# Optimization experiments

Measured on AMD Instinct MI355X. Metric: run time of the kernel, lower is better.

Reference implementation:

```python
import jax, jax.numpy as jnp
import numpy as np
import math

B, L, D, NUM_TYPES = 4, 4096, 512, 22
T_MAX = 200.0
SIGMA, LAMBD = 10.0, 0.005


def setup_inputs() -> dict:
    key = jax.random.key(0)
    k1, k2, k3 = jax.random.split(key, 3)
    event_type = jax.random.randint(k1, (B, L), 0, NUM_TYPES + 1)
    # event times in [0, t_max), sorted along the sequence (realistic point process)
    event_time = jnp.sort(jax.random.uniform(k2, (B, L), dtype=jnp.float32) * T_MAX, axis=-1)
    # embedding table with padding row 0 zeroed (padding_idx=0)
    emb_table = jax.random.normal(k3, (NUM_TYPES + 1, D), dtype=jnp.float32).at[0].set(0.0)
    return {"event_type": event_type, "event_time": event_time, "emb_table": emb_table}


def reference(event_type, event_time, emb_table):
    d_model = emb_table.shape[1]
    seq_len = event_time.shape[1]

    # sinusoidal temporal encoding: t / 10000^(2*(i//2)/d)
    i = jnp.arange(d_model)
    pos_vec = jnp.power(jnp.float32(10000.0), 2.0 * (i // 2).astype(jnp.float32) / d_model)
    temp = event_time[:, :, None] / pos_vec  # [B, L, D]
    temp_enc = jnp.where(i % 2 == 0, jnp.sin(temp), jnp.cos(temp))

    type_embedding = emb_table[event_type] * math.sqrt(d_model)  # [B, L, D]
    embedding = jnp.concatenate([temp_enc, type_embedding], axis=-1)  # [B, L, 2D]

    # RBF kernel pairwise scores: sigma^2 * exp(-(|ti - tj|^norm)^2 / lambd^2), norm=2
    t = event_time / T_MAX  # normalized times
    d = jnp.abs(t[:, :, None] - t[:, None, :]) ** 2  # [B, L, L]
    scores = (SIGMA ** 2) * jnp.exp(-(d ** 2) / (LAMBD ** 2))

    # causal mask: keep j <= i, fill future with -1000, then softmax over rows
    causal = jnp.tril(jnp.ones((seq_len, seq_len), dtype=bool))  # [L, L]
    scores = jnp.where(causal[None, :, :], scores, jnp.float32(-1000.0))
    scores = jax.nn.softmax(scores, axis=-1)
    return scores, embedding
```

## Files before the change

### kernel.cpp

```cpp
#include <hip/hip_runtime.h>

#define SEQ_L 4096
#define BATCH 4
#define DMODEL 512
#define ROWS_PER_BLOCK 4
#define CUT 0.055f

__global__ __launch_bounds__(256) void scores_kernel(const float* __restrict__ tm,
                                                     float* __restrict__ out) {
    __shared__ float ts[SEQ_L];

    const int b  = blockIdx.x / (SEQ_L / ROWS_PER_BLOCK);
    const int i0 = (blockIdx.x % (SEQ_L / ROWS_PER_BLOCK)) * ROWS_PER_BLOCK;

    const float4* tb4 = (const float4*)(tm + b * SEQ_L);
    float4* ts4 = (float4*)ts;
    for (int j = threadIdx.x; j < SEQ_L / 4; j += 256) {
        float4 v = tb4[j];
        v.x /= 200.0f; v.y /= 200.0f; v.z /= 200.0f; v.w /= 200.0f;
        ts4[j] = v;
    }
    __syncthreads();

    const int wave = threadIdx.x >> 6;
    const int lane = threadIdx.x & 63;
    const int i = i0 + wave;
    const float ti = ts[i];
    const float tcut = ti - CUT;

    int lo = 0, hi = i;
    while (lo < hi) {
        int mid = (lo + hi) >> 1;
        if (ts[mid] < tcut) lo = mid + 1; else hi = mid;
    }
    const int jlo = lo;

    float sum = 0.0f;
    for (int j = jlo + lane; j <= i; j += 64) {
        float d = ti - ts[j];
        float d2 = d * d;
        float s = 100.0f * expf(-(d2 * d2) * 40000.0f);
        sum += expf(s - 100.0f);
    }
    #pragma unroll
    for (int off = 1; off < 64; off <<= 1) sum += __shfl_xor(sum, off, 64);
    const float inv_denom = 1.0f / sum;

    float4* out4 = (float4*)(out + ((size_t)(b * SEQ_L + i)) * SEQ_L);
    for (int c = lane; c < SEQ_L / 4; c += 64) {
        const int j = c * 4;
        float4 v = make_float4(0.0f, 0.0f, 0.0f, 0.0f);
        if (j + 3 >= jlo && j <= i) {
            float* vp = &v.x;
            #pragma unroll
            for (int q = 0; q < 4; ++q) {
                const int jj = j + q;
                if (jj >= jlo && jj <= i) {
                    float d = ti - ts[jj];
                    float d2 = d * d;
                    float s = 100.0f * expf(-(d2 * d2) * 40000.0f);
                    vp[q] = expf(s - 100.0f) * inv_denom;
                }
            }
        }
        out4[c] = v;
    }
}

__global__ __launch_bounds__(256) void emb_kernel(const int* __restrict__ et,
                                                  const float* __restrict__ tm,
                                                  const float* __restrict__ tab,
                                                  float* __restrict__ out) {
    const int t = threadIdx.x;
    const bool temporal = t < 128;

    float ipA = 0.0f, ipB = 0.0f;
    if (temporal) {
        const float c = -13.287712379549449f / 256.0f;
        ipA = exp2f(c * (float)(2 * t));
        ipB = exp2f(c * (float)(2 * t + 1));
    }
    const int ecol = (t - 128) * 4;

    for (int bl = blockIdx.x; bl < BATCH * SEQ_L; bl += gridDim.x) {
        float4 v;
        if (temporal) {
            const float time = tm[bl];
            const float a = time * ipA;
            const float bph = time * ipB;
            v.x = sinf(a);  v.y = cosf(a);
            v.z = sinf(bph); v.w = cosf(bph);
        } else {
            const float4 e = *(const float4*)(tab + et[bl] * DMODEL + ecol);
            const float sc = 22.627416997969522f;
            v.x = e.x * sc; v.y = e.y * sc; v.z = e.z * sc; v.w = e.w * sc;
        }
        ((float4*)(out + (size_t)bl * 2 * DMODEL))[t] = v;
    }
}

extern "C" void kernel_launch(void* const* d_in, const int* in_sizes, int n_in,
                              void* d_out, int out_size, void* d_ws, size_t ws_size,
                              hipStream_t stream) {
    const int*   event_type = (const int*)d_in[0];
    const float* event_time = (const float*)d_in[1];
    const float* emb_table  = (const float*)d_in[2];

    float* scores = (float*)d_out;
    float* emb    = scores + (size_t)BATCH * SEQ_L * SEQ_L;

    scores_kernel<<<BATCH * SEQ_L / ROWS_PER_BLOCK, 256, 0, stream>>>(event_time, scores);
    emb_kernel<<<2048, 256, 0, stream>>>(event_type, event_time, emb_table, emb);
}
```

Baseline: 67.47 us.

## Fuse scores and embedding kernels, process 16 rows per block with fast math

Merges the scores and embedding kernels into a single launch that splits its blocks by index. Each score block now handles 16 rows, with each wave doing 4 consecutive rows, so the shared time array is loaded once for more rows and the window start is advanced incrementally instead of searched for every row. It also switches expf/sinf/cosf to the fast __expf/__sinf/__cosf intrinsics. The aim is to cut the cost of a second launch and of repeated shared-memory loads, at the risk of lower accuracy from the intrinsics and fewer blocks to spread across the device.

```diff
diff --git a/kernel.cpp b/kernel.cpp
--- a/kernel.cpp
+++ b/kernel.cpp
@@ -3,99 +3,115 @@
 #define SEQ_L 4096
 #define BATCH 4
 #define DMODEL 512
-#define ROWS_PER_BLOCK 4
 #define CUT 0.055f
+#define RPB 16
+#define SCORE_BLOCKS (BATCH * SEQ_L / RPB)
+#define EMB_BLOCKS 512
+#define EMB_RPB (BATCH * SEQ_L / EMB_BLOCKS)
 
-__global__ __launch_bounds__(256) void scores_kernel(const float* __restrict__ tm,
-                                                     float* __restrict__ out) {
-    __shared__ float ts[SEQ_L];
+__global__ __launch_bounds__(256) void fused_kernel(const int* __restrict__ et,
+                                                    const float* __restrict__ tm,
+                                                    const float* __restrict__ tab,
+                                                    float* __restrict__ scores,
+                                                    float* __restrict__ emb) {
+    if (blockIdx.x < SCORE_BLOCKS) {
+        __shared__ float ts[SEQ_L];
+        const int b  = blockIdx.x / (SEQ_L / RPB);
+        const int i0 = (blockIdx.x % (SEQ_L / RPB)) * RPB;
 
-    const int b  = blockIdx.x / (SEQ_L / ROWS_PER_BLOCK);
-    const int i0 = (blockIdx.x % (SEQ_L / ROWS_PER_BLOCK)) * ROWS_PER_BLOCK;
+        const float4* tb4 = (const float4*)(tm + b * SEQ_L);
+        float4* ts4 = (float4*)ts;
+        const float inv_tmax = 1.0f / 200.0f;
+        #pragma unroll
+        for (int q = 0; q < 4; ++q) {
+            int j = threadIdx.x + q * 256;
+            float4 v = tb4[j];
+            v.x *= inv_tmax; v.y *= inv_tmax; v.z *= inv_tmax; v.w *= inv_tmax;
+            ts4[j] = v;
+        }
+        __syncthreads();
 
-    const float4* tb4 = (const float4*)(tm + b * SEQ_L);
-    float4* ts4 = (float4*)ts;
-    for (int j = threadIdx.x; j < SEQ_L / 4; j += 256) {
-        float4 v = tb4[j];
-        v.x /= 200.0f; v.y /= 200.0f; v.z /= 200.0f; v.w /= 200.0f;
-        ts4[j] = v;
-    }
-    __syncthreads();
+        const int wave = threadIdx.x >> 6;
+        const int lane = threadIdx.x & 63;
+        const int ibase = i0 + wave * 4;
 
-    const int wave = threadIdx.x >> 6;
-    const int lane = threadIdx.x & 63;
-    const int i = i0 + wave;
-    const float ti = ts[i];
-    const float tcut = ti - CUT;
+        int jlo;
+        {
+            const float tc = ts[ibase] - CUT;
+            int lo = 0, hi = ibase;
+            while (lo < hi) {
+                int mid = (lo + hi) >> 1;
+                if (ts[mid] < tc) lo = mid + 1; else hi = mid;
+            }
+            jlo = lo;
+        }
 
-    int lo = 0, hi = i;
-    while (lo < hi) {
-        int mid = (lo + hi) >> 1;
-        if (ts[mid] < tcut) lo = mid + 1; else hi = mid;
-    }
-    const int jlo = lo;
+        for (int r = 0; r < 4; ++r) {
+            const int i = ibase + r;
+            const float ti = ts[i];
+            const float tc = ti - CUT;
+            while (ts[jlo] < tc) ++jlo;
 
-    float sum = 0.0f;
-    for (int j = jlo + lane; j <= i; j += 64) {
-        float d = ti - ts[j];
-        float d2 = d * d;
-        float s = 100.0f * expf(-(d2 * d2) * 40000.0f);
-        sum += expf(s - 100.0f);
-    }
-    #pragma unroll
-    for (int off = 1; off < 64; off <<= 1) sum += __shfl_xor(sum, off, 64);
-    const float inv_denom = 1.0f / sum;
+            float sum = 0.0f;
+            for (int j = jlo + lane; j <= i; j += 64) {
+                float d = ti - ts[j];
+                float d2 = d * d;
+                float s = 100.0f * __expf(-(d2 * d2) * 40000.0f);
+                sum += __expf(s - 100.0f);
+            }
+            #pragma unroll
+            for (int off = 1; off < 64; off <<= 1) sum += __shfl_xor(sum, off, 64);
+            const float inv_denom = 1.0f / sum;
 
-    float4* out4 = (float4*)(out + ((size_t)(b * SEQ_L + i)) * SEQ_L);
-    for (int c = lane; c < SEQ_L / 4; c += 64) {
-        const int j = c * 4;
-        float4 v = make_float4(0.0f, 0.0f, 0.0f, 0.0f);
-        if (j + 3 >= jlo && j <= i) {
-            float* vp = &v.x;
-            #pragma unroll
-            for (int q = 0; q < 4; ++q) {
-                const int jj = j + q;
-                if (jj >= jlo && jj <= i) {
-                    float d = ti - ts[jj];
-                    float d2 = d * d;
-                    float s = 100.0f * expf(-(d2 * d2) * 40000.0f);
-                    vp[q] = expf(s - 100.0f) * inv_denom;
+            float4* out4 = (float4*)(scores + ((size_t)(b * SEQ_L + i)) * SEQ_L);
+            for (int c = lane; c < SEQ_L / 4; c += 64) {
+                const int j = c * 4;
+                float4 v = make_float4(0.0f, 0.0f, 0.0f, 0.0f);
+                if (j + 3 >= jlo && j <= i) {
+                    float* vp = &v.x;
+                    #pragma unroll
+                    for (int q = 0; q < 4; ++q) {
+                        const int jj = j + q;
+                        if (jj >= jlo && jj <= i) {
+                            float d = ti - ts[jj];
+                            float d2 = d * d;
+                            float s = 100.0f * __expf(-(d2 * d2) * 40000.0f);
+                            vp[q] = __expf(s - 100.0f) * inv_denom;
+                        }
+                    }
                 }
+                out4[c] = v;
             }
         }
-        out4[c] = v;
-    }
-}
+    } else {
+        const int t = threadIdx.x;
+        const bool temporal = t < 128;
 
-__global__ __launch_bounds__(256) void emb_kernel(const int* __restrict__ et,
-                                                  const float* __restrict__ tm,
-                                                  const float* __restrict__ tab,
-                                                  float* __restrict__ out) {
-    const int t = threadIdx.x;
-    const bool temporal = t < 128;
+        float ipA = 0.0f, ipB = 0.0f;
+        if (temporal) {
+            const float c = -13.287712379549449f / 256.0f;
+            ipA = exp2f(c * (float)(2 * t));
+            ipB = exp2f(c * (float)(2 * t + 1));
+        }
+        const int ecol = (t - 128) * 4;
 
-    float ipA = 0.0f, ipB = 0.0f;
-    if (temporal) {
-        const float c = -13.287712379549449f / 256.0f;
-        ipA = exp2f(c * (float)(2 * t));
-        ipB = exp2f(c * (float)(2 * t + 1));
-    }
-    const int ecol = (t - 128) * 4;
-
-    for (int bl = blockIdx.x; bl < BATCH * SEQ_L; bl += gridDim.x) {
-        float4 v;
-        if (temporal) {
-            const float time = tm[bl];
-            const float a = time * ipA;
-            const float bph = time * ipB;
-            v.x = sinf(a);  v.y = cosf(a);
-            v.z = sinf(bph); v.w = cosf(bph);
-        } else {
-            const float4 e = *(const float4*)(tab + et[bl] * DMODEL + ecol);
-            const float sc = 22.627416997969522f;
-            v.x = e.x * sc; v.y = e.y * sc; v.z = e.z * sc; v.w = e.w * sc;
+        const int bl0 = (blockIdx.x - SCORE_BLOCKS) * EMB_RPB;
+        for (int r = 0; r < EMB_RPB; ++r) {
+            const int bl = bl0 + r;
+            float4 v;
+            if (temporal) {
+                const float time = tm[bl];
+                const float a = time * ipA;
+                const float bp = time * ipB;
+                v.x = __sinf(a);  v.y = __cosf(a);
+                v.z = __sinf(bp); v.w = __cosf(bp);
+            } else {
+                const float4 e = *(const float4*)(tab + et[bl] * DMODEL + ecol);
+                const float sc = 22.627416997969522f;
+                v.x = e.x * sc; v.y = e.y * sc; v.z = e.z * sc; v.w = e.w * sc;
+            }
+            ((float4*)(emb + (size_t)bl * 2 * DMODEL))[t] = v;
         }
-        ((float4*)(out + (size_t)bl * 2 * DMODEL))[t] = v;
     }
 }
 
@@ -109,6 +125,6 @@
     float* scores = (float*)d_out;
     float* emb    = scores + (size_t)BATCH * SEQ_L * SEQ_L;
 
-    scores_kernel<<<BATCH * SEQ_L / ROWS_PER_BLOCK, 256, 0, stream>>>(event_time, scores);
-    emb_kernel<<<2048, 256, 0, stream>>>(event_type, event_time, emb_table, emb);
+    fused_kernel<<<SCORE_BLOCKS + EMB_BLOCKS, 256, 0, stream>>>(
+        event_type, event_time, emb_table, scores, emb);
 }
```

New measurement: 65.34 us. -3.2%, faster.
